# Kernel optimization log

Measured on AMD Instinct MI355X. Metric: run time of the kernel, lower is better.

## Reference

```python
import jax, jax.numpy as jnp
import numpy as np

ALPHA = 0.2  # LeakyReLU negative slope


def setup_inputs() -> dict:
    key = jax.random.key(0)
    k1, k2 = jax.random.split(key)
    B, N, Fin, Fout = 4, 4096, 256, 128
    h = jax.random.normal(k1, (B, N, Fin), dtype=jnp.float32)
    adj = jnp.zeros((B, N, N), dtype=bool)  # unused by the original forward
    # Linear(in,out,bias=False); stored as [in,out] for h @ W
    W = jax.random.normal(k2, (Fin, Fout), dtype=jnp.float32) * (1.0 / np.sqrt(Fin))
    return {"h": h, "adj": adj, "W": W}


def reference(h, adj, W):
    # h: [B,N,Fin], W: [Fin,Fout]
    hp = jnp.einsum("bnf,fo->bno", h, W)                    # [B,N,Fout]
    e = jnp.einsum("bnd,bmd->bnm", hp, hp)                  # [B,N,N]
    e = jnp.where(e >= 0, e, ALPHA * e)                      # LeakyReLU
    attn = jax.nn.softmax(e, axis=1)                         # softmax over dim=1 (rows)
    # torch: sum_j( hp[b,i] * attn[b,i,j] ) == hp[b,i] * sum_j attn[b,i,j]
    row_mass = jnp.sum(attn, axis=2, keepdims=True)          # [B,N,1]
    return hp * row_mass
```

## Files before the change

kernel.cpp:

```cpp
#include <hip/hip_runtime.h>
#include <hip/hip_bf16.h>

#define ALPHA 0.2f

constexpr int BN   = 4;
constexpr int NN   = 4096;
constexpr int FIN  = 256;
constexpr int FOUT = 128;
constexpr int NQ   = 8;

typedef __attribute__((ext_vector_type(8))) short bf16x8;
typedef __attribute__((ext_vector_type(4))) float f32x4;

#define MFMA16(a, b, c) __builtin_amdgcn_mfma_f32_16x16x32_bf16((a), (b), (c), 0, 0, 0)

__device__ __forceinline__ void split8(const float* x, uint4& H, uint4& L) {
    ushort hb[8], lb[8];
    #pragma unroll
    for (int i = 0; i < 8; ++i) {
        float xv = x[i];
        __hip_bfloat16 hh = __float2bfloat16(xv);
        float hf = __bfloat162float(hh);
        __hip_bfloat16 lw = __float2bfloat16(xv - hf);
        hb[i] = reinterpret_cast<const ushort&>(hh);
        lb[i] = reinterpret_cast<const ushort&>(lw);
    }
    H = make_uint4((uint)hb[0] | ((uint)hb[1] << 16), (uint)hb[2] | ((uint)hb[3] << 16),
                   (uint)hb[4] | ((uint)hb[5] << 16), (uint)hb[6] | ((uint)hb[7] << 16));
    L = make_uint4((uint)lb[0] | ((uint)lb[1] << 16), (uint)lb[2] | ((uint)lb[3] << 16),
                   (uint)lb[4] | ((uint)lb[5] << 16), (uint)lb[6] | ((uint)lb[7] << 16));
}

template<int ROWS, int KGSH>
__device__ __forceinline__ void stage_split(const float* __restrict__ src, int strideF,
                                            ushort* hi, ushort* lo, int tid) {
    constexpr int KG = 1 << KGSH;
    #pragma unroll
    for (int idx = tid; idx < ROWS * KG; idx += 256) {
        int row = idx >> KGSH, g = idx & (KG - 1);
        const float4* p4 = reinterpret_cast<const float4*>(src + (size_t)row * strideF + g * 8);
        float4 u = p4[0], v = p4[1];
        float x[8] = {u.x, u.y, u.z, u.w, v.x, v.y, v.z, v.w};
        uint4 H, L;
        split8(x, H, L);
        int gran = (row << KGSH) + (g ^ (row & 7));
        reinterpret_cast<uint4*>(hi)[gran] = H;
        reinterpret_cast<uint4*>(lo)[gran] = L;
    }
}

template<int ROWS, int KGSH>
__device__ __forceinline__ void stage_copy(const ushort* __restrict__ src, int strideU,
                                           ushort* dst, int tid) {
    constexpr int KG = 1 << KGSH;
    #pragma unroll
    for (int idx = tid; idx < ROWS * KG; idx += 256) {
        int row = idx >> KGSH, g = idx & (KG - 1);
        uint4 vv = *reinterpret_cast<const uint4*>(src + (size_t)row * strideU + g * 8);
        reinterpret_cast<uint4*>(dst)[(row << KGSH) + (g ^ (row & 7))] = vv;
    }
}

__device__ __forceinline__ bf16x8 frag16(const ushort* s, int rowbase, int kstep, int kgsh, int lane) {
    int r = rowbase + (lane & 15);
    int g = kstep * 4 + (lane >> 4);
    int gran = (r << kgsh) + (g ^ (r & 7));
    return *reinterpret_cast<const bf16x8*>(s + gran * 8);
}

__global__ void k_prepW(const float* __restrict__ W, ushort* __restrict__ Wt_hi,
                        ushort* __restrict__ Wt_lo) {
    int idx = blockIdx.x * 256 + threadIdx.x;
    if (idx >= FOUT * (FIN / 8)) return;
    int n = idx >> 5, g = idx & 31;
    float x[8];
    #pragma unroll
    for (int i = 0; i < 8; ++i) x[i] = W[(size_t)(g * 8 + i) * FOUT + n];
    uint4 H, L;
    split8(x, H, L);
    reinterpret_cast<uint4*>(Wt_hi)[n * 32 + g] = H;
    reinterpret_cast<uint4*>(Wt_lo)[n * 32 + g] = L;
}

__global__ __launch_bounds__(256)
void k_hp(const float* __restrict__ h, const ushort* __restrict__ Wt_hi,
          const ushort* __restrict__ Wt_lo, float* __restrict__ hp,
          ushort* __restrict__ hp_hi, ushort* __restrict__ hp_lo) {
    __shared__ __align__(16) ushort Ah[64 * 64], Al[64 * 64];
    __shared__ __align__(16) ushort Bh[128 * 64], Bl[128 * 64];
    const int tid = threadIdx.x, lane = tid & 63, wid = tid >> 6;
    const int wy = wid >> 1, wx = wid & 1;
    const int ibase = blockIdx.x * 64;
    f32x4 z = {0.f, 0.f, 0.f, 0.f};
    f32x4 acc[2][4] = {{z, z, z, z}, {z, z, z, z}};
    for (int kt = 0; kt < 4; ++kt) {
        __syncthreads();
        stage_split<64, 3>(h + (size_t)ibase * FIN + kt * 64, FIN, Ah, Al, tid);
        stage_copy<128, 3>(Wt_hi + kt * 64, FIN, Bh, tid);
        stage_copy<128, 3>(Wt_lo + kt * 64, FIN, Bl, tid);
        __syncthreads();
        #pragma unroll
        for (int pr = 0; pr < 3; ++pr) {
            const ushort* A = (pr == 2) ? Al : Ah;
            const ushort* B = (pr == 1) ? Bl : Bh;
            #pragma unroll
            for (int ks = 0; ks < 2; ++ks) {
                bf16x8 a0 = frag16(A, wy * 32, ks, 3, lane);
                bf16x8 a1 = frag16(A, wy * 32 + 16, ks, 3, lane);
                #pragma unroll
                for (int c = 0; c < 4; ++c) {
                    bf16x8 bb = frag16(B, wx * 64 + c * 16, ks, 3, lane);
                    acc[0][c] = MFMA16(a0, bb, acc[0][c]);
                    acc[1][c] = MFMA16(a1, bb, acc[1][c]);
                }
            }
        }
    }
    #pragma unroll
    for (int r = 0; r < 2; ++r)
        #pragma unroll
        for (int c = 0; c < 4; ++c)
            #pragma unroll
            for (int p = 0; p < 4; ++p) {
                int row = ibase + wy * 32 + r * 16 + (lane >> 4) * 4 + p;
                int col = wx * 64 + c * 16 + (lane & 15);
                float x = acc[r][c][p];
                __hip_bfloat16 hh = __float2bfloat16(x);
                float hf = __bfloat162float(hh);
                __hip_bfloat16 lw = __float2bfloat16(x - hf);
                size_t off = (size_t)row * FOUT + col;
                hp[off] = x;
                hp_hi[off] = reinterpret_cast<const ushort&>(hh);
                hp_lo[off] = reinterpret_cast<const ushort&>(lw);
            }
}

__device__ __forceinline__ void etile44(const ushort* Ihi, const ushort* Ilo,
                                        const ushort* Jhi, const ushort* Jlo,
                                        int wy, int wx, int lane, f32x4 acc[4][4]) {
    #pragma unroll
    for (int ks = 0; ks < 4; ++ks) {
        bf16x8 aH[4], aL[4], bH[4], bL[4];
        #pragma unroll
        for (int r = 0; r < 4; ++r) {
            aH[r] = frag16(Ihi, wy * 64 + r * 16, ks, 4, lane);
            aL[r] = frag16(Ilo, wy * 64 + r * 16, ks, 4, lane);
        }
        #pragma unroll
        for (int c = 0; c < 4; ++c) {
            bH[c] = frag16(Jhi, wx * 64 + c * 16, ks, 4, lane);
            bL[c] = frag16(Jlo, wx * 64 + c * 16, ks, 4, lane);
        }
        #pragma unroll
        for (int r = 0; r < 4; ++r)
            #pragma unroll
            for (int c = 0; c < 4; ++c) {
                acc[r][c] = MFMA16(aH[r], bH[c], acc[r][c]);
                acc[r][c] = MFMA16(aH[r], bL[c], acc[r][c]);
                acc[r][c] = MFMA16(aL[r], bH[c], acc[r][c]);
            }
    }
}

__device__ __forceinline__ void decode_bid(int bid, int& b, int& strip, int& q) {
    int slot = bid & 7;
    b = slot >> 1;
    int sub = ((bid >> 3) << 1) | (slot & 1);
    strip = sub >> 3;
    q = sub & 7;
}

__global__ __launch_bounds__(256)
void k_colstats(const ushort* __restrict__ hp_hi, const ushort* __restrict__ hp_lo,
                float* __restrict__ m_part, float* __restrict__ s_part) {
    __shared__ __align__(16) ushort Jhi[128 * 128], Jlo[128 * 128];
    __shared__ __align__(16) ushort Ihi[128 * 128], Ilo[128 * 128];
    const int tid = threadIdx.x, lane = tid & 63, wid = tid >> 6;
    const int wy = wid >> 1, wx = wid & 1;
    int b, strip, q;
    decode_bid(blockIdx.x, b, strip, q);
    const int jbase = strip * 128;
    const ushort* hb_hi = hp_hi + (size_t)b * NN * FOUT;
    const ushort* hb_lo = hp_lo + (size_t)b * NN * FOUT;
    stage_copy<128, 4>(hb_hi + (size_t)jbase * FOUT, FOUT, Jhi, tid);
    stage_copy<128, 4>(hb_lo + (size_t)jbase * FOUT, FOUT, Jlo, tid);
    float mrun[4] = {-1e30f, -1e30f, -1e30f, -1e30f};
    float srun[4] = {0.f, 0.f, 0.f, 0.f};
    for (int t = 0; t < 4; ++t) {
        int ibase = q * 512 + t * 128;
        __syncthreads();
        stage_copy<128, 4>(hb_hi + (size_t)ibase * FOUT, FOUT, Ihi, tid);
        stage_copy<128, 4>(hb_lo + (size_t)ibase * FOUT, FOUT, Ilo, tid);
        __syncthreads();
        f32x4 zz = {0.f, 0.f, 0.f, 0.f};
        f32x4 acc[4][4];
        #pragma unroll
        for (int r = 0; r < 4; ++r)
            #pragma unroll
            for (int c = 0; c < 4; ++c) acc[r][c] = zz;
        etile44(Ihi, Ilo, Jhi, Jlo, wy, wx, lane, acc);
        #pragma unroll
        for (int c = 0; c < 4; ++c) {
            float tm = -1e30f;
            #pragma unroll
            for (int r = 0; r < 4; ++r)
                #pragma unroll
                for (int p = 0; p < 4; ++p) {
                    float x = acc[r][c][p];
                    float g = fmaxf(x, ALPHA * x);
                    acc[r][c][p] = g;
                    tm = fmaxf(tm, g);
                }
            tm = fmaxf(tm, __shfl_xor(tm, 16));
            tm = fmaxf(tm, __shfl_xor(tm, 32));
            float mnew = fmaxf(mrun[c], tm);
            float ss = 0.f;
            #pragma unroll
            for (int r = 0; r < 4; ++r)
                #pragma unroll
                for (int p = 0; p < 4; ++p) ss += __expf(acc[r][c][p] - mnew);
            ss += __shfl_xor(ss, 16);
            ss += __shfl_xor(ss, 32);
            srun[c] = srun[c] * __expf(mrun[c] - mnew) + ss;
            mrun[c] = mnew;
        }
    }
    if (lane < 16) {
        int set = b * 16 + q * 2 + wy;
        #pragma unroll
        for (int c = 0; c < 4; ++c) {
            int j = jbase + wx * 64 + c * 16 + lane;
            m_part[(size_t)set * NN + j] = mrun[c];
            s_part[(size_t)set * NN + j] = srun[c];
        }
    }
}

__global__ void k_merge(const float* __restrict__ m_part, const float* __restrict__ s_part,
                        float* __restrict__ m_fin, float* __restrict__ inv_s) {
    int idx = blockIdx.x * 256 + threadIdx.x;
    if (idx >= BN * NN) return;
    int b = idx >> 12, j = idx & (NN - 1);
    float M = -1e30f;
    #pragma unroll
    for (int k = 0; k < 16; ++k)
        M = fmaxf(M, m_part[(size_t)(b * 16 + k) * NN + j]);
    float S = 0.f;
    #pragma unroll
    for (int k = 0; k < 16; ++k) {
        float mp = m_part[(size_t)(b * 16 + k) * NN + j];
        float sp = s_part[(size_t)(b * 16 + k) * NN + j];
        S += sp * __expf(mp - M);
    }
    m_fin[idx] = M;
    inv_s[idx] = 1.f / S;
}

__global__ __launch_bounds__(256)
void k_rowsum(const ushort* __restrict__ hp_hi, const ushort* __restrict__ hp_lo,
              const float* __restrict__ m_fin, const float* __restrict__ inv_s,
              float* __restrict__ rs_part) {
    __shared__ __align__(16) ushort Ihi[128 * 128], Ilo[128 * 128];
    __shared__ __align__(16) ushort Jhi[128 * 128], Jlo[128 * 128];
    __shared__ float red[128][2];
    const int tid = threadIdx.x, lane = tid & 63, wid = tid >> 6;
    const int wy = wid >> 1, wx = wid & 1;
    int b, strip, jq;
    decode_bid(blockIdx.x, b, strip, jq);
    const int ibase = strip * 128;
    const ushort* hb_hi = hp_hi + (size_t)b * NN * FOUT;
    const ushort* hb_lo = hp_lo + (size_t)b * NN * FOUT;
    stage_copy<128, 4>(hb_hi + (size_t)ibase * FOUT, FOUT, Ihi, tid);
    stage_copy<128, 4>(hb_lo + (size_t)ibase * FOUT, FOUT, Ilo, tid);
    float rsum[4][4] = {};
    for (int t = 0; t < 4; ++t) {
        int jb = jq * 512 + t * 128;
        __syncthreads();
        stage_copy<128, 4>(hb_hi + (size_t)jb * FOUT, FOUT, Jhi, tid);
        stage_copy<128, 4>(hb_lo + (size_t)jb * FOUT, FOUT, Jlo, tid);
        __syncthreads();
        float mj[4], isj[4];
        #pragma unroll
        for (int c = 0; c < 4; ++c) {
            int j = jb + wx * 64 + c * 16 + (lane & 15);
            mj[c] = m_fin[(size_t)b * NN + j];
            isj[c] = inv_s[(size_t)b * NN + j];
        }
        f32x4 zz = {0.f, 0.f, 0.f, 0.f};
        f32x4 acc[4][4];
        #pragma unroll
        for (int r = 0; r < 4; ++r)
            #pragma unroll
            for (int c = 0; c < 4; ++c) acc[r][c] = zz;
        etile44(Ihi, Ilo, Jhi, Jlo, wy, wx, lane, acc);
        #pragma unroll
        for (int r = 0; r < 4; ++r)
            #pragma unroll
            for (int p = 0; p < 4; ++p) {
                float s0 = 0.f;
                #pragma unroll
                for (int c = 0; c < 4; ++c) {
                    float x = acc[r][c][p];
                    float g = fmaxf(x, ALPHA * x);
                    s0 += __expf(g - mj[c]) * isj[c];
                }
                rsum[r][p] += s0;
            }
    }
    #pragma unroll
    for (int r = 0; r < 4; ++r)
        #pragma unroll
        for (int p = 0; p < 4; ++p) {
            float v = rsum[r][p];
            v += __shfl_xor(v, 1);
            v += __shfl_xor(v, 2);
            v += __shfl_xor(v, 4);
            v += __shfl_xor(v, 8);
            if ((lane & 15) == 0) red[wy * 64 + r * 16 + (lane >> 4) * 4 + p][wx] = v;
        }
    __syncthreads();
    if (tid < 128)
        rs_part[(size_t)(b * NQ + jq) * NN + ibase + tid] = red[tid][0] + red[tid][1];
}

__global__ void k_scale(const float* __restrict__ rs_part, float* __restrict__ out) {
    int idx = blockIdx.x * 256 + threadIdx.x;
    if (idx >= BN * NN * FOUT / 4) return;
    int row = idx >> 5;
    int b = row >> 12, i = row & (NN - 1);
    float rm = 0.f;
    #pragma unroll
    for (int k = 0; k < NQ; ++k)
        rm += rs_part[(size_t)(b * NQ + k) * NN + i];
    float4 v = reinterpret_cast<float4*>(out)[idx];
    v.x *= rm; v.y *= rm; v.z *= rm; v.w *= rm;
    reinterpret_cast<float4*>(out)[idx] = v;
}

extern "C" void kernel_launch(void* const* d_in, const int* in_sizes, int n_in,
                              void* d_out, int out_size, void* d_ws, size_t ws_size,
                              hipStream_t stream) {
    (void)in_sizes; (void)n_in; (void)out_size; (void)ws_size;
    const float* h = (const float*)d_in[0];
    const float* W = (const float*)d_in[2];
    float* out = (float*)d_out;
    ushort* hp_hi = (ushort*)d_ws;
    ushort* hp_lo = hp_hi + (size_t)BN * NN * FOUT;
    ushort* Wt_hi = hp_lo + (size_t)BN * NN * FOUT;
    ushort* Wt_lo = Wt_hi + FOUT * FIN;
    float* m_part = (float*)(Wt_lo + FOUT * FIN);
    float* s_part = m_part + (size_t)BN * 16 * NN;
    float* m_fin  = s_part + (size_t)BN * 16 * NN;
    float* inv_s  = m_fin + (size_t)BN * NN;
    float* rs_part = inv_s + (size_t)BN * NN;

    k_prepW<<<(FOUT * (FIN / 8) + 255) / 256, 256, 0, stream>>>(W, Wt_hi, Wt_lo);
    k_hp<<<BN * NN / 64, 256, 0, stream>>>(h, Wt_hi, Wt_lo, out, hp_hi, hp_lo);
    k_colstats<<<BN * NQ * (NN / 128), 256, 0, stream>>>(hp_hi, hp_lo, m_part, s_part);
    k_merge<<<(BN * NN + 255) / 256, 256, 0, stream>>>(m_part, s_part, m_fin, inv_s);
    k_rowsum<<<BN * NQ * (NN / 128), 256, 0, stream>>>(hp_hi, hp_lo, m_fin, inv_s, rs_part);
    k_scale<<<(BN * NN * FOUT / 4 + 255) / 256, 256, 0, stream>>>(rs_part, out);
}
```

Baseline: 498.5 us.

## Exploit symmetry of hp·hpᵀ: compute upper-triangle tiles once, use for rows and columns

Because e = hp·hpᵀ is symmetric, the stats and mass kernels now process only upper-triangular 64x64 tile pairs, one per wavefront. Each tile contributes both its row and its transposed column partials, roughly halving the MFMA work. Operands are read straight from global memory instead of staged through LDS, and row reductions use DPP. The trade-off is more partial buffers (64 per batch) to merge, extra exp work on the transposed side, and a loop-based task decode.

```diff
diff --git a/kernel.cpp b/kernel.cpp
--- a/kernel.cpp
+++ b/kernel.cpp
@@ -7,12 +7,33 @@
 constexpr int NN   = 4096;
 constexpr int FIN  = 256;
 constexpr int FOUT = 128;
-constexpr int NQ   = 8;
+constexpr int NT   = 64;
+constexpr int NPAIR = NT * (NT + 1) / 2;
 
 typedef __attribute__((ext_vector_type(8))) short bf16x8;
 typedef __attribute__((ext_vector_type(4))) float f32x4;
 
 #define MFMA16(a, b, c) __builtin_amdgcn_mfma_f32_16x16x32_bf16((a), (b), (c), 0, 0, 0)
+
+template<int CTRL>
+__device__ __forceinline__ float dpp_mov(float x) {
+    return __int_as_float(__builtin_amdgcn_update_dpp(
+        __float_as_int(x), __float_as_int(x), CTRL, 0xF, 0xF, false));
+}
+__device__ __forceinline__ float rsum16(float x) {
+    x += dpp_mov<0x128>(x);
+    x += dpp_mov<0x124>(x);
+    x += dpp_mov<0x122>(x);
+    x += dpp_mov<0x121>(x);
+    return x;
+}
+__device__ __forceinline__ float rmax16(float x) {
+    x = fmaxf(x, dpp_mov<0x128>(x));
+    x = fmaxf(x, dpp_mov<0x124>(x));
+    x = fmaxf(x, dpp_mov<0x122>(x));
+    x = fmaxf(x, dpp_mov<0x121>(x));
+    return x;
+}
 
 __device__ __forceinline__ void split8(const float* x, uint4& H, uint4& L) {
     ushort hb[8], lb[8];
@@ -48,7 +69,6 @@
         reinterpret_cast<uint4*>(lo)[gran] = L;
     }
 }
-
 template<int ROWS, int KGSH>
 __device__ __forceinline__ void stage_copy(const ushort* __restrict__ src, int strideU,
                                            ushort* dst, int tid) {
@@ -60,7 +80,6 @@
         reinterpret_cast<uint4*>(dst)[(row << KGSH) + (g ^ (row & 7))] = vv;
     }
 }
-
 __device__ __forceinline__ bf16x8 frag16(const ushort* s, int rowbase, int kstep, int kgsh, int lane) {
     int r = rowbase + (lane & 15);
     int g = kstep * 4 + (lane >> 4);
@@ -135,103 +154,111 @@
             }
 }
 
-__device__ __forceinline__ void etile44(const ushort* Ihi, const ushort* Ilo,
-                                        const ushort* Jhi, const ushort* Jlo,
-                                        int wy, int wx, int lane, f32x4 acc[4][4]) {
+__device__ __forceinline__ void decode_task(int task, int& b, int& ti, int& tj) {
+    b = task / NPAIR;
+    int sub = task - b * NPAIR;
+    int t = 0, width = NT;
+    while (sub >= width) { sub -= width; --width; ++t; }
+    ti = t;
+    tj = t + sub;
+}
+
+__device__ __forceinline__ void etile_g(const ushort* __restrict__ Hh,
+                                        const ushort* __restrict__ Hl,
+                                        int ibase, int jbase, int lane,
+                                        f32x4 acc[4][4]) {
+    const int lrow = lane & 15, lg = lane >> 4;
     #pragma unroll
     for (int ks = 0; ks < 4; ++ks) {
-        bf16x8 aH[4], aL[4], bH[4], bL[4];
+        const int g8 = (ks * 4 + lg) * 8;
+        bf16x8 aH[4], aL[4];
         #pragma unroll
         for (int r = 0; r < 4; ++r) {
-            aH[r] = frag16(Ihi, wy * 64 + r * 16, ks, 4, lane);
-            aL[r] = frag16(Ilo, wy * 64 + r * 16, ks, 4, lane);
+            size_t off = (size_t)(ibase + r * 16 + lrow) * FOUT + g8;
+            aH[r] = *reinterpret_cast<const bf16x8*>(Hh + off);
+            aL[r] = *reinterpret_cast<const bf16x8*>(Hl + off);
         }
         #pragma unroll
         for (int c = 0; c < 4; ++c) {
-            bH[c] = frag16(Jhi, wx * 64 + c * 16, ks, 4, lane);
-            bL[c] = frag16(Jlo, wx * 64 + c * 16, ks, 4, lane);
-        }
+            size_t off = (size_t)(jbase + c * 16 + lrow) * FOUT + g8;
+            bf16x8 bH = *reinterpret_cast<const bf16x8*>(Hh + off);
+            bf16x8 bL = *reinterpret_cast<const bf16x8*>(Hl + off);
+            #pragma unroll
+            for (int r = 0; r < 4; ++r) {
+                acc[r][c] = MFMA16(aH[r], bH, acc[r][c]);
+                acc[r][c] = MFMA16(aH[r], bL, acc[r][c]);
+                acc[r][c] = MFMA16(aL[r], bH, acc[r][c]);
+            }
+        }
+    }
+}
+
+__global__ __launch_bounds__(256)
+void k_stats(const ushort* __restrict__ hp_hi, const ushort* __restrict__ hp_lo,
+             float* __restrict__ m_part, float* __restrict__ s_part) {
+    const int tid = threadIdx.x, lane = tid & 63, wid = tid >> 6;
+    const int lrow = lane & 15, lg = lane >> 4;
+    int b, ti, tj;
+    decode_task(blockIdx.x * 4 + wid, b, ti, tj);
+    const size_t bo = (size_t)b * NN * FOUT;
+    const int ibase = ti * 64, jbase = tj * 64;
+    f32x4 z = {0.f, 0.f, 0.f, 0.f};
+    f32x4 acc[4][4] = {{z,z,z,z},{z,z,z,z},{z,z,z,z},{z,z,z,z}};
+    etile_g(hp_hi + bo, hp_lo + bo, ibase, jbase, lane, acc);
+    #pragma unroll
+    for (int r = 0; r < 4; ++r)
+        #pragma unroll
+        for (int c = 0; c < 4; ++c)
+            #pragma unroll
+            for (int p = 0; p < 4; ++p) {
+                float x = acc[r][c][p];
+                acc[r][c][p] = fmaxf(x, ALPHA * x);
+            }
+    {
+        float* mp = m_part + (size_t)(b * NT + tj) * NN;
+        float* sp = s_part + (size_t)(b * NT + tj) * NN;
         #pragma unroll
         for (int r = 0; r < 4; ++r)
             #pragma unroll
-            for (int c = 0; c < 4; ++c) {
-                acc[r][c] = MFMA16(aH[r], bH[c], acc[r][c]);
-                acc[r][c] = MFMA16(aH[r], bL[c], acc[r][c]);
-                acc[r][c] = MFMA16(aL[r], bH[c], acc[r][c]);
-            }
-    }
-}
-
-__device__ __forceinline__ void decode_bid(int bid, int& b, int& strip, int& q) {
-    int slot = bid & 7;
-    b = slot >> 1;
-    int sub = ((bid >> 3) << 1) | (slot & 1);
-    strip = sub >> 3;
-    q = sub & 7;
-}
-
-__global__ __launch_bounds__(256)
-void k_colstats(const ushort* __restrict__ hp_hi, const ushort* __restrict__ hp_lo,
-                float* __restrict__ m_part, float* __restrict__ s_part) {
-    __shared__ __align__(16) ushort Jhi[128 * 128], Jlo[128 * 128];
-    __shared__ __align__(16) ushort Ihi[128 * 128], Ilo[128 * 128];
-    const int tid = threadIdx.x, lane = tid & 63, wid = tid >> 6;
-    const int wy = wid >> 1, wx = wid & 1;
-    int b, strip, q;
-    decode_bid(blockIdx.x, b, strip, q);
-    const int jbase = strip * 128;
-    const ushort* hb_hi = hp_hi + (size_t)b * NN * FOUT;
-    const ushort* hb_lo = hp_lo + (size_t)b * NN * FOUT;
-    stage_copy<128, 4>(hb_hi + (size_t)jbase * FOUT, FOUT, Jhi, tid);
-    stage_copy<128, 4>(hb_lo + (size_t)jbase * FOUT, FOUT, Jlo, tid);
-    float mrun[4] = {-1e30f, -1e30f, -1e30f, -1e30f};
-    float srun[4] = {0.f, 0.f, 0.f, 0.f};
-    for (int t = 0; t < 4; ++t) {
-        int ibase = q * 512 + t * 128;
-        __syncthreads();
-        stage_copy<128, 4>(hb_hi + (size_t)ibase * FOUT, FOUT, Ihi, tid);
-        stage_copy<128, 4>(hb_lo + (size_t)ibase * FOUT, FOUT, Ilo, tid);
-        __syncthreads();
-        f32x4 zz = {0.f, 0.f, 0.f, 0.f};
-        f32x4 acc[4][4];
-        #pragma unroll
-        for (int r = 0; r < 4; ++r)
-            #pragma unroll
-            for (int c = 0; c < 4; ++c) acc[r][c] = zz;
-        etile44(Ihi, Ilo, Jhi, Jlo, wy, wx, lane, acc);
+            for (int p = 0; p < 4; ++p) {
+                float mx = fmaxf(fmaxf(acc[r][0][p], acc[r][1][p]),
+                                 fmaxf(acc[r][2][p], acc[r][3][p]));
+                mx = rmax16(mx);
+                float se = 0.f;
+                #pragma unroll
+                for (int c = 0; c < 4; ++c) se += __expf(acc[r][c][p] - mx);
+                se = rsum16(se);
+                if (lrow == 0) {
+                    int i = ibase + r * 16 + lg * 4 + p;
+                    mp[i] = mx;
+                    sp[i] = se;
+                }
+            }
+    }
+    if (ti != tj) {
+        float* mp = m_part + (size_t)(b * NT + ti) * NN;
+        float* sp = s_part + (size_t)(b * NT + ti) * NN;
         #pragma unroll
         for (int c = 0; c < 4; ++c) {
-            float tm = -1e30f;
+            float mx = -1e30f;
             #pragma unroll
             for (int r = 0; r < 4; ++r)
                 #pragma unroll
-                for (int p = 0; p < 4; ++p) {
-                    float x = acc[r][c][p];
-                    float g = fmaxf(x, ALPHA * x);
-                    acc[r][c][p] = g;
-                    tm = fmaxf(tm, g);
-                }
-            tm = fmaxf(tm, __shfl_xor(tm, 16));
-            tm = fmaxf(tm, __shfl_xor(tm, 32));
-            float mnew = fmaxf(mrun[c], tm);
-            float ss = 0.f;
+                for (int p = 0; p < 4; ++p) mx = fmaxf(mx, acc[r][c][p]);
+            mx = fmaxf(mx, __shfl_xor(mx, 16));
+            mx = fmaxf(mx, __shfl_xor(mx, 32));
+            float se = 0.f;
             #pragma unroll
             for (int r = 0; r < 4; ++r)
                 #pragma unroll
-                for (int p = 0; p < 4; ++p) ss += __expf(acc[r][c][p] - mnew);
-            ss += __shfl_xor(ss, 16);
-            ss += __shfl_xor(ss, 32);
-            srun[c] = srun[c] * __expf(mrun[c] - mnew) + ss;
-            mrun[c] = mnew;
-        }
-    }
-    if (lane < 16) {
-        int set = b * 16 + q * 2 + wy;
-        #pragma unroll
-        for (int c = 0; c < 4; ++c) {
-            int j = jbase + wx * 64 + c * 16 + lane;
-            m_part[(size_t)set * NN + j] = mrun[c];
-            s_part[(size_t)set * NN + j] = srun[c];
+                for (int p = 0; p < 4; ++p) se += __expf(acc[r][c][p] - mx);
+            se += __shfl_xor(se, 16);
+            se += __shfl_xor(se, 32);
+            if (lane < 16) {
+                int j = jbase + c * 16 + lane;
+                mp[j] = mx;
+                sp[j] = se;
+            }
         }
     }
 }
@@ -240,87 +267,83 @@
                         float* __restrict__ m_fin, float* __restrict__ inv_s) {
     int idx = blockIdx.x * 256 + threadIdx.x;
     if (idx >= BN * NN) return;
-    int b = idx >> 12, j = idx & (NN - 1);
+    int b = idx >> 12, row = idx & (NN - 1);
+    const float* mp = m_part + (size_t)b * NT * NN + row;
+    const float* sp = s_part + (size_t)b * NT * NN + row;
     float M = -1e30f;
-    #pragma unroll
-    for (int k = 0; k < 16; ++k)
-        M = fmaxf(M, m_part[(size_t)(b * 16 + k) * NN + j]);
+    for (int k = 0; k < NT; ++k) M = fmaxf(M, mp[(size_t)k * NN]);
     float S = 0.f;
-    #pragma unroll
-    for (int k = 0; k < 16; ++k) {
-        float mp = m_part[(size_t)(b * 16 + k) * NN + j];
-        float sp = s_part[(size_t)(b * 16 + k) * NN + j];
-        S += sp * __expf(mp - M);
-    }
+    for (int k = 0; k < NT; ++k) S += sp[(size_t)k * NN] * __expf(mp[(size_t)k * NN] - M);
     m_fin[idx] = M;
     inv_s[idx] = 1.f / S;
 }
 
 __global__ __launch_bounds__(256)
-void k_rowsum(const ushort* __restrict__ hp_hi, const ushort* __restrict__ hp_lo,
-              const float* __restrict__ m_fin, const float* __restrict__ inv_s,
-              float* __restrict__ rs_part) {
-    __shared__ __align__(16) ushort Ihi[128 * 128], Ilo[128 * 128];
-    __shared__ __align__(16) ushort Jhi[128 * 128], Jlo[128 * 128];
-    __shared__ float red[128][2];
+void k_mass(const ushort* __restrict__ hp_hi, const ushort* __restrict__ hp_lo,
+            const float* __restrict__ m_fin, const float* __restrict__ inv_s,
+            float* __restrict__ rs_part) {
     const int tid = threadIdx.x, lane = tid & 63, wid = tid >> 6;
-    const int wy = wid >> 1, wx = wid & 1;
-    int b, strip, jq;
-    decode_bid(blockIdx.x, b, strip, jq);
-    const int ibase = strip * 128;
-    const ushort* hb_hi = hp_hi + (size_t)b * NN * FOUT;
-    const ushort* hb_lo = hp_lo + (size_t)b * NN * FOUT;
-    stage_copy<128, 4>(hb_hi + (size_t)ibase * FOUT, FOUT, Ihi, tid);
-    stage_copy<128, 4>(hb_lo + (size_t)ibase * FOUT, FOUT, Ilo, tid);
-    float rsum[4][4] = {};
-    for (int t = 0; t < 4; ++t) {
-        int jb = jq * 512 + t * 128;
-        __syncthreads();
-        stage_copy<128, 4>(hb_hi + (size_t)jb * FOUT, FOUT, Jhi, tid);
-        stage_copy<128, 4>(hb_lo + (size_t)jb * FOUT, FOUT, Jlo, tid);
-        __syncthreads();
-        float mj[4], isj[4];
-        #pragma unroll
-        for (int c = 0; c < 4; ++c) {
-            int j = jb + wx * 64 + c * 16 + (lane & 15);
-            mj[c] = m_fin[(size_t)b * NN + j];
-            isj[c] = inv_s[(size_t)b * NN + j];
-        }
-        f32x4 zz = {0.f, 0.f, 0.f, 0.f};
-        f32x4 acc[4][4];
+    const int lrow = lane & 15, lg = lane >> 4;
+    int b, ti, tj;
+    decode_task(blockIdx.x * 4 + wid, b, ti, tj);
+    const size_t bo = (size_t)b * NN * FOUT;
+    const int ibase = ti * 64, jbase = tj * 64;
+    f32x4 z = {0.f, 0.f, 0.f, 0.f};
+    f32x4 acc[4][4] = {{z,z,z,z},{z,z,z,z},{z,z,z,z},{z,z,z,z}};
+    etile_g(hp_hi + bo, hp_lo + bo, ibase, jbase, lane, acc);
+    const float* mf = m_fin + (size_t)b * NN;
+    const float* isv = inv_s + (size_t)b * NN;
+    float mj[4], sj[4];
+    #pragma unroll
+    for (int c = 0; c < 4; ++c) {
+        int j = jbase + c * 16 + lrow;
+        mj[c] = mf[j];
+        sj[c] = isv[j];
+    }
+    {
+        float* rs = rs_part + (size_t)(b * NT + tj) * NN;
         #pragma unroll
         for (int r = 0; r < 4; ++r)
             #pragma unroll
-            for (int c = 0; c < 4; ++c) acc[r][c] = zz;
-        etile44(Ihi, Ilo, Jhi, Jlo, wy, wx, lane, acc);
-        #pragma unroll
-        for (int r = 0; r < 4; ++r)
-            #pragma unroll
-            for (int p = 0; p < 4; ++p) {
-                float s0 = 0.f;
+            for (int p = 0; p < 4; ++p) {
+                float s = 0.f;
                 #pragma unroll
                 for (int c = 0; c < 4; ++c) {
                     float x = acc[r][c][p];
                     float g = fmaxf(x, ALPHA * x);
-                    s0 += __expf(g - mj[c]) * isj[c];
+                    s += __expf(g - mj[c]) * sj[c];
                 }
-                rsum[r][p] += s0;
-            }
-    }
-    #pragma unroll
-    for (int r = 0; r < 4; ++r)
-        #pragma unroll
-        for (int p = 0; p < 4; ++p) {
-            float v = rsum[r][p];
-            v += __shfl_xor(v, 1);
-            v += __shfl_xor(v, 2);
-            v += __shfl_xor(v, 4);
-            v += __shfl_xor(v, 8);
-            if ((lane & 15) == 0) red[wy * 64 + r * 16 + (lane >> 4) * 4 + p][wx] = v;
-        }
-    __syncthreads();
-    if (tid < 128)
-        rs_part[(size_t)(b * NQ + jq) * NN + ibase + tid] = red[tid][0] + red[tid][1];
+                s = rsum16(s);
+                if (lrow == 0) rs[ibase + r * 16 + lg * 4 + p] = s;
+            }
+    }
+    if (ti != tj) {
+        float mi[4][4], si_[4][4];
+        #pragma unroll
+        for (int r = 0; r < 4; ++r)
+            #pragma unroll
+            for (int p = 0; p < 4; ++p) {
+                int i = ibase + r * 16 + lg * 4 + p;
+                mi[r][p] = mf[i];
+                si_[r][p] = isv[i];
+            }
+        float* rs = rs_part + (size_t)(b * NT + ti) * NN;
+        #pragma unroll
+        for (int c = 0; c < 4; ++c) {
+            float s2 = 0.f;
+            #pragma unroll
+            for (int r = 0; r < 4; ++r)
+                #pragma unroll
+                for (int p = 0; p < 4; ++p) {
+                    float x = acc[r][c][p];
+                    float g = fmaxf(x, ALPHA * x);
+                    s2 += __expf(g - mi[r][p]) * si_[r][p];
+                }
+            s2 += __shfl_xor(s2, 16);
+            s2 += __shfl_xor(s2, 32);
+            if (lane < 16) rs[jbase + c * 16 + lane] = s2;
+        }
+    }
 }
 
 __global__ void k_scale(const float* __restrict__ rs_part, float* __restrict__ out) {
@@ -328,10 +351,9 @@
     if (idx >= BN * NN * FOUT / 4) return;
     int row = idx >> 5;
     int b = row >> 12, i = row & (NN - 1);
+    const float* rs = rs_part + (size_t)b * NT * NN + i;
     float rm = 0.f;
-    #pragma unroll
-    for (int k = 0; k < NQ; ++k)
-        rm += rs_part[(size_t)(b * NQ + k) * NN + i];
+    for (int k = 0; k < NT; ++k) rm += rs[(size_t)k * NN];
     float4 v = reinterpret_cast<float4*>(out)[idx];
     v.x *= rm; v.y *= rm; v.z *= rm; v.w *= rm;
     reinterpret_cast<float4*>(out)[idx] = v;
@@ -349,15 +371,15 @@
     ushort* Wt_hi = hp_lo + (size_t)BN * NN * FOUT;
     ushort* Wt_lo = Wt_hi + FOUT * FIN;
     float* m_part = (float*)(Wt_lo + FOUT * FIN);
-    float* s_part = m_part + (size_t)BN * 16 * NN;
-    float* m_fin  = s_part + (size_t)BN * 16 * NN;
+    float* s_part = m_part + (size_t)BN * NT * NN;
+    float* m_fin  = s_part + (size_t)BN * NT * NN;
     float* inv_s  = m_fin + (size_t)BN * NN;
     float* rs_part = inv_s + (size_t)BN * NN;
 
     k_prepW<<<(FOUT * (FIN / 8) + 255) / 256, 256, 0, stream>>>(W, Wt_hi, Wt_lo);
     k_hp<<<BN * NN / 64, 256, 0, stream>>>(h, Wt_hi, Wt_lo, out, hp_hi, hp_lo);
-    k_colstats<<<BN * NQ * (NN / 128), 256, 0, stream>>>(hp_hi, hp_lo, m_part, s_part);
+    k_stats<<<BN * NPAIR / 4, 256, 0, stream>>>(hp_hi, hp_lo, m_part, s_part);
     k_merge<<<(BN * NN + 255) / 256, 256, 0, stream>>>(m_part, s_part, m_fin, inv_s);
-    k_rowsum<<<BN * NQ * (NN / 128), 256, 0, stream>>>(hp_hi, hp_lo, m_fin, inv_s, rs_part);
+    k_mass<<<BN * NPAIR / 4, 256, 0, stream>>>(hp_hi, hp_lo, m_fin, inv_s, rs_part);
     k_scale<<<(BN * NN * FOUT / 4 + 255) / 256, 256, 0, stream>>>(rs_part, out);
 }
```

After: 503.8 us. No clear change (+1.1%).
